# Kernel tuning notes

Measured on AMD Instinct MI355X. Metric: run time of the kernel, lower is better.

## Reference

```python
import jax, jax.numpy as jnp
import numpy as np

N, E, H = 100000, 640000, 64
DIN_N, DIN_E, L, OUT = 32, 16, 2, 1
BN_EPS = 1e-5


def setup_inputs() -> dict:
    key = jax.random.key(0)
    ks = iter(jax.random.split(key, 40))
    def p(shape, s=0.05):
        return jax.random.normal(next(ks), shape, dtype=jnp.float32) * s
    return {
        "x": jax.random.normal(next(ks), (N, DIN_N), dtype=jnp.float32),
        "edge_attr": jax.random.normal(next(ks), (E, DIN_E), dtype=jnp.float32),
        "src": jax.random.randint(next(ks), (E,), 0, N),
        "dst": jax.random.randint(next(ks), (E,), 0, N),
        "node_emb_w": p((DIN_N, H)), "node_emb_b": p((H,)),
        "edge_emb_w": p((DIN_E, H)), "edge_emb_b": p((H,)),
        "lin_edge_w": p((L, H, H)), "lin_edge_b": p((L, H)),
        "conv_w1": p((L, H, H)), "conv_b1": p((L, H)),
        "conv_w2": p((L, H, H)), "conv_b2": p((L, H)),
        "emlp_w1": p((L, 3 * H, H)), "emlp_b1": p((L, H)),
        "emlp_w2": p((L, H, H)), "emlp_b2": p((L, H)),
        "bn_gamma": jnp.ones((L, H), jnp.float32),
        "bn_beta": jnp.zeros((L, H), jnp.float32),
        "mlp_w1": p((3 * H, 50)), "mlp_b1": p((50,)),
        "mlp_w2": p((50, 25)), "mlp_b2": p((25,)),
        "mlp_w3": p((25, OUT)), "mlp_b3": p((OUT,)),
    }


def _batchnorm(h, gamma, beta):
    # training-mode BatchNorm1d over the node axis (biased variance)
    mu = jnp.mean(h, axis=0)
    var = jnp.mean(jnp.square(h - mu), axis=0)
    return gamma * (h - mu) * jax.lax.rsqrt(var + BN_EPS) + beta


def _forward(x, edge_attr, src, dst,
             node_emb_w, node_emb_b, edge_emb_w, edge_emb_b,
             lin_edge_w, lin_edge_b, conv_w1, conv_b1, conv_w2, conv_b2,
             emlp_w1, emlp_b1, emlp_w2, emlp_b2, bn_gamma, bn_beta,
             mlp_w1, mlp_b1, mlp_w2, mlp_b2, mlp_w3, mlp_b3):
    x = x @ node_emb_w + node_emb_b                       # [N, H]
    e = edge_attr @ edge_emb_w + edge_emb_b               # [E, H]
    for i in range(L):
        # GINEConv (eps=0): msg = ReLU(x_src + Lin(edge_attr)); sum at dst
        msg = jax.nn.relu(x[src] + e @ lin_edge_w[i] + lin_edge_b[i])
        agg = jax.ops.segment_sum(msg, dst, num_segments=N)
        h = x + agg
        h = jax.nn.relu(h @ conv_w1[i] + conv_b1[i]) @ conv_w2[i] + conv_b2[i]
        x = (x + jax.nn.relu(_batchnorm(h, bn_gamma[i], bn_beta[i]))) / 2
        cat = jnp.concatenate([x[src], x[dst], e], axis=-1)  # [E, 3H]
        upd = jax.nn.relu(cat @ emlp_w1[i] + emlp_b1[i]) @ emlp_w2[i] + emlp_b2[i]
        e = e + upd / 2
    # edge readout: relu(cat(x_src, x_dst)) ++ edge_attr -> MLP (dropout off/eval)
    er = jnp.concatenate(
        [jax.nn.relu(jnp.concatenate([x[src], x[dst]], axis=-1)), e], axis=-1)
    hmid = jax.nn.relu(er @ mlp_w1 + mlp_b1)
    hmid = jax.nn.relu(hmid @ mlp_w2 + mlp_b2)
    logit = hmid @ mlp_w3 + mlp_b3
    return x, logit


def reference(x, edge_attr, src, dst,
              node_emb_w, node_emb_b, edge_emb_w, edge_emb_b,
              lin_edge_w, lin_edge_b, conv_w1, conv_b1, conv_w2, conv_b2,
              emlp_w1, emlp_b1, emlp_w2, emlp_b2, bn_gamma, bn_beta,
              mlp_w1, mlp_b1, mlp_w2, mlp_b2, mlp_w3, mlp_b3):
    return _forward(x, edge_attr, src, dst,
                    node_emb_w, node_emb_b, edge_emb_w, edge_emb_b,
                    lin_edge_w, lin_edge_b, conv_w1, conv_b1, conv_w2, conv_b2,
                    emlp_w1, emlp_b1, emlp_w2, emlp_b2, bn_gamma, bn_beta,
                    mlp_w1, mlp_b1, mlp_w2, mlp_b2, mlp_w3, mlp_b3)
```

## Files before the change

kernel.cpp:

```cpp
#include <hip/hip_runtime.h>

#define NN 100000
#define NE 640000
#define NB_SCAN 98

typedef __attribute__((ext_vector_type(8))) short short8;
typedef __attribute__((ext_vector_type(4))) float f32x4;
typedef __attribute__((ext_vector_type(4))) ushort ushort4v;

__device__ __forceinline__ float bf2f(ushort u) {
    unsigned v = ((unsigned)u) << 16;
    return __builtin_bit_cast(float, v);
}
__device__ __forceinline__ ushort f2bf(float f) {
    unsigned u = __builtin_bit_cast(unsigned, f);
    u += 0x7fffu + ((u >> 16) & 1u);
    return (ushort)(u >> 16);
}
__device__ __forceinline__ short8 brelu(short8 v) {
    #pragma unroll
    for (int i = 0; i < 8; ++i) v[i] = (v[i] < (short)0) ? (short)0 : v[i];
    return v;
}

__global__ void k_hist(const int* __restrict__ dst, int* __restrict__ hist)
{
    int i = blockIdx.x * 256 + threadIdx.x;
    atomicAdd(&hist[dst[i]], 1);
}

__global__ __launch_bounds__(256) void k_scan_part(const int* __restrict__ hist,
                                                   int* __restrict__ rp,
                                                   int* __restrict__ parts)
{
    __shared__ int s[256];
    int b = blockIdx.x, t = threadIdx.x;
    int base = b * 1024 + t * 4;
    int v[4]; int sum = 0;
    #pragma unroll
    for (int i = 0; i < 4; ++i) { int idx = base + i; v[i] = (idx < NN) ? hist[idx] : 0; sum += v[i]; }
    s[t] = sum; __syncthreads();
    for (int off = 1; off < 256; off <<= 1) {
        int x = (t >= off) ? s[t - off] : 0;
        __syncthreads(); s[t] += x; __syncthreads();
    }
    int excl = s[t] - sum;
    if (t == 255) parts[b] = s[255];
    int run = excl;
    #pragma unroll
    for (int i = 0; i < 4; ++i) { int idx = base + i; if (idx < NN) rp[idx] = run; run += v[i]; }
}

__global__ void k_scan_tops(int* __restrict__ parts, int* __restrict__ rp)
{
    __shared__ int s[128];
    int t = threadIdx.x;
    int v = (t < NB_SCAN) ? parts[t] : 0;
    s[t] = v; __syncthreads();
    for (int off = 1; off < 128; off <<= 1) {
        int x = (t >= off) ? s[t - off] : 0;
        __syncthreads(); s[t] += x; __syncthreads();
    }
    parts[t] = s[t] - v;
    if (t == 0) rp[NN] = NE;
}

__global__ __launch_bounds__(256) void k_scan_add(int* __restrict__ rp,
                                                  const int* __restrict__ parts,
                                                  int* __restrict__ cursor)
{
    int i = blockIdx.x * 256 + threadIdx.x;
    if (i >= NN) return;
    int v = rp[i] + parts[i >> 10];
    rp[i] = v; cursor[i] = v;
}

__global__ void k_scatter(const int* __restrict__ dst,
                          int* __restrict__ cursor, int* __restrict__ eidx)
{
    int i = blockIdx.x * 256 + threadIdx.x;
    int d = dst[i];
    int p = atomicAdd(&cursor[d], 1);
    eidx[p] = i;
}

__global__ void k_w_subtile(const float* __restrict__ w, ushort* __restrict__ out,
                            int K, int Nin)
{
    int t = blockIdx.x * 256 + threadIdx.x;
    if (t >= K * 64) return;
    int k = t >> 6, c = t & 63;
    float v = (c < Nin) ? w[k * Nin + c] : 0.f;
    out[((k >> 3) * 64 + c) * 8 + (k & 7)] = f2bf(v);
}

__global__ void k_w_padk(const float* __restrict__ w, ushort* __restrict__ out,
                         int Kreal, int Kpad)
{
    int t = blockIdx.x * 256 + threadIdx.x;
    if (t >= Kpad * 64) return;
    int k = t >> 6, c = t & 63;
    float v = (k < Kreal) ? w[k * 64 + c] : 0.f;
    out[((k >> 3) * 64 + c) * 8 + (k & 7)] = f2bf(v);
}

__global__ void k_w_msg(const float* __restrict__ lw, ushort* __restrict__ out)
{
    int t = blockIdx.x * 256 + threadIdx.x;
    if (t >= 128 * 64) return;
    int k = t >> 6, c = t & 63;
    float v = (k < 64) ? (k == c ? 1.f : 0.f) : lw[(k - 64) * 64 + c];
    out[((k >> 3) * 64 + c) * 8 + (k & 7)] = f2bf(v);
}

__global__ __launch_bounds__(256) void k_node_emb_mfma(
    const float* __restrict__ xin, const ushort* __restrict__ ws,
    const float* __restrict__ b, float* __restrict__ xout,
    ushort* __restrict__ xb)
{
    __shared__ ushort wl[32 * 64];
    __shared__ float fbuf[4][16 * 64];
    __shared__ ushort bbuf[4][16 * 64];
    int tid = threadIdx.x;
    *(short8*)&wl[tid * 8] = *(const short8*)&ws[tid * 8];
    __syncthreads();

    int wid = tid >> 6, lane = tid & 63, c = lane & 15, kg = lane >> 4;
    int t = blockIdx.x * 4 + wid;
    if (t >= NN / 16) return;
    int n0 = t * 16;

    const float* xr = xin + (size_t)(n0 + c) * 32 + kg * 8;
    f32x4 u0 = *(const f32x4*)xr, u1 = *(const f32x4*)(xr + 4);
    short8 a;
    #pragma unroll
    for (int j = 0; j < 4; ++j) { a[j] = (short)f2bf(u0[j]); a[4 + j] = (short)f2bf(u1[j]); }

    f32x4 acc[4];
    #pragma unroll
    for (int nt = 0; nt < 4; ++nt) {
        float bv = b[nt * 16 + c];
        acc[nt] = f32x4{bv, bv, bv, bv};
        short8 bf = *(const short8*)&wl[(kg * 64 + nt * 16 + c) * 8];
        acc[nt] = __builtin_amdgcn_mfma_f32_16x16x32_bf16(a, bf, acc[nt], 0, 0, 0);
    }
    #pragma unroll
    for (int nt = 0; nt < 4; ++nt)
        #pragma unroll
        for (int i = 0; i < 4; ++i) {
            int rr = kg * 4 + i, cc = nt * 16 + c;
            float v = acc[nt][i];
            fbuf[wid][rr * 64 + cc] = v;
            bbuf[wid][rr * 64 + cc] = f2bf(v);
        }
    #pragma unroll
    for (int r = 0; r < 4; ++r) {
        int q = r * 64 + lane;
        *(f32x4*)&xout[(size_t)(n0 + (q >> 4)) * 64 + (q & 15) * 4] =
            *(f32x4*)&fbuf[wid][q * 4];
    }
    #pragma unroll
    for (int r = 0; r < 2; ++r) {
        int q = r * 64 + lane;
        *(short8*)&xb[(size_t)(n0 + (q >> 3)) * 64 + (q & 7) * 8] =
            *(short8*)&bbuf[wid][q * 8];
    }
}

__global__ __launch_bounds__(256) void k_edge_emb_fused(
    const float* __restrict__ ein, const ushort* __restrict__ ws,
    const float* __restrict__ b, ushort* __restrict__ eb,
    const ushort* __restrict__ xb, const int* __restrict__ src,
    const ushort* __restrict__ wm, const float* __restrict__ lb,
    ushort* __restrict__ msgbuf)
{
    __shared__ ushort wl[32 * 64];
    __shared__ ushort wml[128 * 64];
    __shared__ ushort bbuf[4][16 * 72];
    int tid = threadIdx.x;
    *(short8*)&wl[tid * 8] = *(const short8*)&ws[tid * 8];
    #pragma unroll
    for (int i = 0; i < 4; ++i)
        *(short8*)&wml[(i * 256 + tid) * 8] = *(const short8*)&wm[(i * 256 + tid) * 8];
    __syncthreads();

    int wid = tid >> 6, lane = tid & 63, c = lane & 15, kg = lane >> 4;
    int e0 = (blockIdx.x * 4 + wid) * 16;
    ushort* bb = bbuf[wid];

    const ushort* xs = xb + (size_t)src[e0 + c] * 64;
    short8 a0 = *(const short8*)(xs + kg * 8);
    short8 a1 = *(const short8*)(xs + 32 + kg * 8);

    short8 a = (short8)0;
    if (kg < 2) {
        const float* er = ein + (size_t)(e0 + c) * 16 + kg * 8;
        f32x4 u0 = *(const f32x4*)er, u1 = *(const f32x4*)(er + 4);
        #pragma unroll
        for (int j = 0; j < 4; ++j) { a[j] = (short)f2bf(u0[j]); a[4 + j] = (short)f2bf(u1[j]); }
    }
    f32x4 acc[4];
    #pragma unroll
    for (int nt = 0; nt < 4; ++nt) {
        float bv = b[nt * 16 + c];
        acc[nt] = f32x4{bv, bv, bv, bv};
        short8 bf = *(const short8*)&wl[(kg * 64 + nt * 16 + c) * 8];
        acc[nt] = __builtin_amdgcn_mfma_f32_16x16x32_bf16(a, bf, acc[nt], 0, 0, 0);
    }
    #pragma unroll
    for (int nt = 0; nt < 4; ++nt)
        #pragma unroll
        for (int i = 0; i < 4; ++i)
            bb[(kg * 4 + i) * 72 + nt * 16 + c] = f2bf(acc[nt][i]);
    #pragma unroll
    for (int r = 0; r < 2; ++r) {
        int q = r * 64 + lane;
        *(short8*)&eb[(size_t)(e0 + (q >> 3)) * 64 + (q & 7) * 8] =
            *(short8*)&bb[(q >> 3) * 72 + (q & 7) * 8];
    }
    short8 en0 = *(const short8*)&bb[c * 72 + kg * 8];
    short8 en1 = *(const short8*)&bb[c * 72 + 32 + kg * 8];

    f32x4 acc3[4];
    #pragma unroll
    for (int nt = 0; nt < 4; ++nt) {
        float bv = lb[nt * 16 + c];
        acc3[nt] = f32x4{bv, bv, bv, bv};
    }
    short8 af[4] = {a0, a1, en0, en1};
    #pragma unroll
    for (int ks = 0; ks < 4; ++ks) {
        #pragma unroll
        for (int nt = 0; nt < 4; ++nt) {
            short8 bf = *(const short8*)&wml[((ks * 4 + kg) * 64 + nt * 16 + c) * 8];
            acc3[nt] = __builtin_amdgcn_mfma_f32_16x16x32_bf16(af[ks], bf, acc3[nt], 0, 0, 0);
        }
    }
    #pragma unroll
    for (int nt = 0; nt < 4; ++nt)
        #pragma unroll
        for (int i = 0; i < 4; ++i)
            bb[(kg * 4 + i) * 72 + nt * 16 + c] = f2bf(fmaxf(acc3[nt][i], 0.f));
    #pragma unroll
    for (int r = 0; r < 2; ++r) {
        int q = r * 64 + lane;
        *(short8*)&msgbuf[(size_t)(e0 + (q >> 3)) * 64 + (q & 7) * 8] =
            *(short8*)&bb[(q >> 3) * 72 + (q & 7) * 8];
    }
}

__global__ __launch_bounds__(256) void k_conv_csr(
    const float* __restrict__ x, const ushort* __restrict__ msgbuf,
    const int* __restrict__ rp, const int* __restrict__ eidx,
    float* __restrict__ hout,
    const ushort* __restrict__ w1s, const float* __restrict__ b1,
    const ushort* __restrict__ w2s, const float* __restrict__ b2,
    float* __restrict__ stats)
{
    __shared__ ushort w1l[64 * 64];
    __shared__ ushort w2l[64 * 64];
    __shared__ ushort h1l[4][1024];
    __shared__ float red[2][4][64];
    int tid = threadIdx.x;
    #pragma unroll
    for (int i = 0; i < 2; ++i) {
        *(short8*)&w1l[(i * 256 + tid) * 8] = *(const short8*)&w1s[(i * 256 + tid) * 8];
        *(short8*)&w2l[(i * 256 + tid) * 8] = *(const short8*)&w2s[(i * 256 + tid) * 8];
    }
    __syncthreads();

    int wid = tid >> 6, lane = tid & 63;
    int c = lane & 15, kg = lane >> 4;

    short8 w2f[2][4];
    #pragma unroll
    for (int ks = 0; ks < 2; ++ks)
        #pragma unroll
        for (int nt = 0; nt < 4; ++nt)
            w2f[ks][nt] = *(const short8*)&w2l[((ks * 4 + kg) * 64 + nt * 16 + c) * 8];

    float b1v[4], b2v[4];
    #pragma unroll
    for (int nt = 0; nt < 4; ++nt) { b1v[nt] = b1[nt * 16 + c]; b2v[nt] = b2[nt * 16 + c]; }

    float s1[4] = {0.f, 0.f, 0.f, 0.f}, s2[4] = {0.f, 0.f, 0.f, 0.f};
    ushort* hl = h1l[wid];

    int t = blockIdx.x * 4 + wid;
    if (t < NN / 16) {
        int n0 = t * 16;
        int n = n0 + c;
        int jb = rp[n], je = rp[n + 1];
        float sm0[8] = {0,0,0,0,0,0,0,0}, sm1[8] = {0,0,0,0,0,0,0,0};
        if (jb < je) {
            int row = eidx[jb];
            short8 m0 = *(const short8*)&msgbuf[(size_t)row * 64 + kg * 8];
            short8 m1 = *(const short8*)&msgbuf[(size_t)row * 64 + 32 + kg * 8];
            for (int j = jb + 1; j <= je; ++j) {
                short8 p0, p1;
                if (j < je) {
                    int nrow = eidx[j];
                    p0 = *(const short8*)&msgbuf[(size_t)nrow * 64 + kg * 8];
                    p1 = *(const short8*)&msgbuf[(size_t)nrow * 64 + 32 + kg * 8];
                }
                #pragma unroll
                for (int i = 0; i < 8; ++i) {
                    sm0[i] += bf2f((ushort)m0[i]);
                    sm1[i] += bf2f((ushort)m1[i]);
                }
                if (j < je) { m0 = p0; m1 = p1; }
            }
        }
        const float* xr = x + (size_t)n * 64;
        f32x4 u0 = *(const f32x4*)(xr + kg * 8);
        f32x4 u1 = *(const f32x4*)(xr + kg * 8 + 4);
        f32x4 v0 = *(const f32x4*)(xr + 32 + kg * 8);
        f32x4 v1 = *(const f32x4*)(xr + 32 + kg * 8 + 4);
        short8 a[2];
        #pragma unroll
        for (int j = 0; j < 4; ++j) {
            a[0][j]     = (short)f2bf(u0[j] + sm0[j]);
            a[0][4 + j] = (short)f2bf(u1[j] + sm0[4 + j]);
            a[1][j]     = (short)f2bf(v0[j] + sm1[j]);
            a[1][4 + j] = (short)f2bf(v1[j] + sm1[4 + j]);
        }
        f32x4 acc[4];
        #pragma unroll
        for (int nt = 0; nt < 4; ++nt) acc[nt] = f32x4{b1v[nt], b1v[nt], b1v[nt], b1v[nt]};
        #pragma unroll
        for (int ks = 0; ks < 2; ++ks) {
            #pragma unroll
            for (int nt = 0; nt < 4; ++nt) {
                short8 bf = *(const short8*)&w1l[((ks * 4 + kg) * 64 + nt * 16 + c) * 8];
                acc[nt] = __builtin_amdgcn_mfma_f32_16x16x32_bf16(a[ks], bf, acc[nt], 0, 0, 0);
            }
        }
        #pragma unroll
        for (int nt = 0; nt < 4; ++nt) {
            #pragma unroll
            for (int i = 0; i < 4; ++i) {
                int rr = kg * 4 + i, cc = nt * 16 + c;
                hl[((cc >> 3) * 16 + rr) * 8 + (cc & 7)] = f2bf(fmaxf(acc[nt][i], 0.f));
            }
        }
        f32x4 acc2[4];
        #pragma unroll
        for (int nt = 0; nt < 4; ++nt) acc2[nt] = f32x4{b2v[nt], b2v[nt], b2v[nt], b2v[nt]};
        #pragma unroll
        for (int ks = 0; ks < 2; ++ks) {
            short8 ha = *(const short8*)&hl[((ks * 4 + kg) * 16 + c) * 8];
            #pragma unroll
            for (int nt = 0; nt < 4; ++nt)
                acc2[nt] = __builtin_amdgcn_mfma_f32_16x16x32_bf16(ha, w2f[ks][nt], acc2[nt], 0, 0, 0);
        }
        #pragma unroll
        for (int nt = 0; nt < 4; ++nt) {
            #pragma unroll
            for (int i = 0; i < 4; ++i) {
                int rr = kg * 4 + i, cc = nt * 16 + c;
                float h2 = acc2[nt][i];
                hout[(size_t)(n0 + rr) * 64 + cc] = h2;
                s1[nt] += h2;
                s2[nt] += h2 * h2;
            }
        }
    }
    #pragma unroll
    for (int nt = 0; nt < 4; ++nt) {
        float v1 = s1[nt], v2 = s2[nt];
        v1 += __shfl_xor(v1, 16); v1 += __shfl_xor(v1, 32);
        v2 += __shfl_xor(v2, 16); v2 += __shfl_xor(v2, 32);
        s1[nt] = v1; s2[nt] = v2;
    }
    if (lane < 16) {
        #pragma unroll
        for (int nt = 0; nt < 4; ++nt) {
            red[0][wid][nt * 16 + c] = s1[nt];
            red[1][wid][nt * 16 + c] = s2[nt];
        }
    }
    __syncthreads();
    if (wid == 0) {
        float a = red[0][0][lane] + red[0][1][lane] + red[0][2][lane] + red[0][3][lane];
        float b = red[1][0][lane] + red[1][1][lane] + red[1][2][lane] + red[1][3][lane];
        unsafeAtomicAdd(&stats[lane], a);
        unsafeAtomicAdd(&stats[64 + lane], b);
    }
}

__global__ void k_bnfin(float* __restrict__ stats,
                        const float* __restrict__ gamma,
                        const float* __restrict__ beta)
{
    int j = threadIdx.x;
    float mu = stats[j] * (1.f / NN);
    float var = stats[64 + j] * (1.f / NN) - mu * mu;
    float a = gamma[j] * rsqrtf(var + 1e-5f);
    stats[128 + j] = a;
    stats[192 + j] = beta[j] - mu * a;
}

__global__ __launch_bounds__(256) void k_xupd4(float* __restrict__ x,
                                               const float* __restrict__ h,
                                               const float* __restrict__ stats,
                                               ushort* __restrict__ xb)
{
    int idx = blockIdx.x * 256 + threadIdx.x;
    int j4 = (idx & 15) * 4;
    f32x4 hv = *(const f32x4*)&h[(size_t)idx * 4];
    f32x4 xv = *(const f32x4*)&x[(size_t)idx * 4];
    f32x4 av = *(const f32x4*)&stats[128 + j4];
    f32x4 cv = *(const f32x4*)&stats[192 + j4];
    f32x4 xo;
    ushort4v bo;
    #pragma unroll
    for (int i = 0; i < 4; ++i) {
        float r = fmaxf(fmaf(hv[i], av[i], cv[i]), 0.f);
        float xn = (xv[i] + r) * 0.5f;
        xo[i] = xn;
        bo[i] = f2bf(xn);
    }
    *(f32x4*)&x[(size_t)idx * 4] = xo;
    *(ushort4v*)&xb[(size_t)idx * 4] = bo;
}

template<int NEXT>
__global__ __launch_bounds__(256) void k_emlp_fused(
    const ushort* __restrict__ xb, ushort* __restrict__ eb,
    const int* __restrict__ src, const int* __restrict__ dst,
    const ushort* __restrict__ w1s, const float* __restrict__ b1,
    const ushort* __restrict__ w2s, const float* __restrict__ b2,
    const ushort* __restrict__ wm, const float* __restrict__ lbn,
    ushort* __restrict__ msgbuf)
{
    __shared__ ushort w1l[192 * 64];
    __shared__ ushort wml[NEXT ? 128 * 64 : 8];
    __shared__ ushort hb[4][1152];
    int tid = threadIdx.x;
    #pragma unroll
    for (int i = 0; i < 6; ++i)
        *(short8*)&w1l[(i * 256 + tid) * 8] = *(const short8*)&w1s[(i * 256 + tid) * 8];
    if (NEXT) {
        #pragma unroll
        for (int i = 0; i < 4; ++i)
            *(short8*)&wml[(i * 256 + tid) * 8] = *(const short8*)&wm[(i * 256 + tid) * 8];
    }
    __syncthreads();

    int wid = tid >> 6, lane = tid & 63;
    int c = lane & 15, kg = lane >> 4;

    short8 w2f[2][4];
    #pragma unroll
    for (int ks = 0; ks < 2; ++ks)
        #pragma unroll
        for (int nt = 0; nt < 4; ++nt)
            w2f[ks][nt] = *(const short8*)&w2s[((ks * 4 + kg) * 64 + nt * 16 + c) * 8];

    float b1v[4], b2v[4], lbv[4];
    #pragma unroll
    for (int nt = 0; nt < 4; ++nt) {
        b1v[nt] = b1[nt * 16 + c];
        b2v[nt] = b2[nt * 16 + c];
        lbv[nt] = NEXT ? lbn[nt * 16 + c] : 0.f;
    }
    ushort* hl = hb[wid];

    int ebase = blockIdx.x * 256 + wid * 64;

    short8 a[6];
    {
        int myedge = ebase + c;
        int s = src[myedge], d = dst[myedge];
        const ushort* xs = xb + (size_t)s * 64;
        const ushort* xd = xb + (size_t)d * 64;
        const ushort* ee = eb + (size_t)myedge * 64;
        a[0] = *(const short8*)(xs + kg * 8);
        a[1] = *(const short8*)(xs + 32 + kg * 8);
        a[2] = *(const short8*)(xd + kg * 8);
        a[3] = *(const short8*)(xd + 32 + kg * 8);
        a[4] = *(const short8*)(ee + kg * 8);
        a[5] = *(const short8*)(ee + 32 + kg * 8);
    }

    #pragma unroll 1
    for (int t4 = 0; t4 < 4; ++t4) {
        int e0 = ebase + t4 * 16;
        int myedge = e0 + c;

        short8 an[6];
        if (t4 < 3) {
            int sn = src[myedge + 16];
            int dn = dst[myedge + 16];
            const ushort* xsn = xb + (size_t)sn * 64;
            const ushort* xdn = xb + (size_t)dn * 64;
            const ushort* een = eb + (size_t)(myedge + 16) * 64;
            an[0] = *(const short8*)(xsn + kg * 8);
            an[1] = *(const short8*)(xsn + 32 + kg * 8);
            an[2] = *(const short8*)(xdn + kg * 8);
            an[3] = *(const short8*)(xdn + 32 + kg * 8);
            an[4] = *(const short8*)(een + kg * 8);
            an[5] = *(const short8*)(een + 32 + kg * 8);
        }

        f32x4 acc[4];
        #pragma unroll
        for (int nt = 0; nt < 4; ++nt) acc[nt] = f32x4{b1v[nt], b1v[nt], b1v[nt], b1v[nt]};
        #pragma unroll
        for (int ks = 0; ks < 6; ++ks) {
            #pragma unroll
            for (int nt = 0; nt < 4; ++nt) {
                short8 bf = *(const short8*)&w1l[((ks * 4 + kg) * 64 + nt * 16 + c) * 8];
                acc[nt] = __builtin_amdgcn_mfma_f32_16x16x32_bf16(a[ks], bf, acc[nt], 0, 0, 0);
            }
        }
        #pragma unroll
        for (int nt = 0; nt < 4; ++nt) {
            #pragma unroll
            for (int i = 0; i < 4; ++i) {
                int rr = kg * 4 + i, cc = nt * 16 + c;
                hl[((cc >> 3) * 16 + rr) * 8 + (cc & 7)] = f2bf(fmaxf(acc[nt][i], 0.f));
            }
        }
        f32x4 acc2[4];
        #pragma unroll
        for (int nt = 0; nt < 4; ++nt) acc2[nt] = f32x4{b2v[nt], b2v[nt], b2v[nt], b2v[nt]};
        #pragma unroll
        for (int ks = 0; ks < 2; ++ks) {
            short8 ha = *(const short8*)&hl[((ks * 4 + kg) * 16 + c) * 8];
            #pragma unroll
            for (int nt = 0; nt < 4; ++nt)
                acc2[nt] = __builtin_amdgcn_mfma_f32_16x16x32_bf16(ha, w2f[ks][nt], acc2[nt], 0, 0, 0);
        }
        #pragma unroll
        for (int nt = 0; nt < 4; ++nt)
            #pragma unroll
            for (int i = 0; i < 4; ++i)
                hl[(kg * 4 + i) * 72 + nt * 16 + c] = f2bf(acc2[nt][i]);
        short8 u0 = *(const short8*)&hl[c * 72 + kg * 8];
        short8 u1 = *(const short8*)&hl[c * 72 + 32 + kg * 8];
        short8 en0, en1;
        #pragma unroll
        for (int j = 0; j < 8; ++j) {
            en0[j] = (short)f2bf(bf2f((ushort)a[4][j]) + 0.5f * bf2f((ushort)u0[j]));
            en1[j] = (short)f2bf(bf2f((ushort)a[5][j]) + 0.5f * bf2f((ushort)u1[j]));
        }
        *(short8*)&eb[(size_t)myedge * 64 + kg * 8]      = en0;
        *(short8*)&eb[(size_t)myedge * 64 + 32 + kg * 8] = en1;

        if (NEXT) {
            f32x4 acc3[4];
            #pragma unroll
            for (int nt = 0; nt < 4; ++nt) acc3[nt] = f32x4{lbv[nt], lbv[nt], lbv[nt], lbv[nt]};
            short8 af[4] = {a[0], a[1], en0, en1};
            #pragma unroll
            for (int ks = 0; ks < 4; ++ks) {
                #pragma unroll
                for (int nt = 0; nt < 4; ++nt) {
                    short8 bf = *(const short8*)&wml[((ks * 4 + kg) * 64 + nt * 16 + c) * 8];
                    acc3[nt] = __builtin_amdgcn_mfma_f32_16x16x32_bf16(af[ks], bf, acc3[nt], 0, 0, 0);
                }
            }
            #pragma unroll
            for (int nt = 0; nt < 4; ++nt)
                #pragma unroll
                for (int i = 0; i < 4; ++i)
                    hl[(kg * 4 + i) * 72 + nt * 16 + c] = f2bf(fmaxf(acc3[nt][i], 0.f));
            #pragma unroll
            for (int r = 0; r < 2; ++r) {
                int q = r * 64 + lane;
                *(short8*)&msgbuf[(size_t)(e0 + (q >> 3)) * 64 + (q & 7) * 8] =
                    *(short8*)&hl[(q >> 3) * 72 + (q & 7) * 8];
            }
        }

        if (t4 < 3) {
            #pragma unroll
            for (int i = 0; i < 6; ++i) a[i] = an[i];
        }
    }
}

__global__ __launch_bounds__(256) void k_readout_mfma(
    const ushort* __restrict__ xb, const ushort* __restrict__ eb,
    const int* __restrict__ src, const int* __restrict__ dst,
    const ushort* __restrict__ w1s, const float* __restrict__ b1,
    const float* __restrict__ w2, const float* __restrict__ b2,
    const float* __restrict__ w3, const float* __restrict__ b3,
    float* __restrict__ logit)
{
    __shared__ ushort w1l[192 * 64];
    __shared__ ushort hw[4][64 * 50];
    int tid = threadIdx.x;
    #pragma unroll
    for (int i = 0; i < 6; ++i)
        *(short8*)&w1l[(i * 256 + tid) * 8] = *(const short8*)&w1s[(i * 256 + tid) * 8];
    __syncthreads();

    int wid = tid >> 6, lane = tid & 63;
    int c = lane & 15, kg = lane >> 4;
    float b1v[4];
    #pragma unroll
    for (int nt = 0; nt < 4; ++nt) b1v[nt] = (nt * 16 + c < 50) ? b1[nt * 16 + c] : 0.f;

    int ebase = blockIdx.x * 256 + wid * 64;

    short8 a[6];
    {
        int myedge = ebase + c;
        int s = src[myedge], d = dst[myedge];
        const ushort* xs = xb + (size_t)s * 64;
        const ushort* xd = xb + (size_t)d * 64;
        const ushort* ee = eb + (size_t)myedge * 64;
        a[0] = *(const short8*)(xs + kg * 8);
        a[1] = *(const short8*)(xs + 32 + kg * 8);
        a[2] = *(const short8*)(xd + kg * 8);
        a[3] = *(const short8*)(xd + 32 + kg * 8);
        a[4] = *(const short8*)(ee + kg * 8);
        a[5] = *(const short8*)(ee + 32 + kg * 8);
    }

    #pragma unroll 1
    for (int t4 = 0; t4 < 4; ++t4) {
        int e0 = ebase + t4 * 16;
        int myedge = e0 + c;

        short8 an[6];
        if (t4 < 3) {
            int sn = src[myedge + 16];
            int dn = dst[myedge + 16];
            const ushort* xsn = xb + (size_t)sn * 64;
            const ushort* xdn = xb + (size_t)dn * 64;
            const ushort* een = eb + (size_t)(myedge + 16) * 64;
            an[0] = *(const short8*)(xsn + kg * 8);
            an[1] = *(const short8*)(xsn + 32 + kg * 8);
            an[2] = *(const short8*)(xdn + kg * 8);
            an[3] = *(const short8*)(xdn + 32 + kg * 8);
            an[4] = *(const short8*)(een + kg * 8);
            an[5] = *(const short8*)(een + 32 + kg * 8);
        }

        short8 af[6];
        af[0] = brelu(a[0]); af[1] = brelu(a[1]);
        af[2] = brelu(a[2]); af[3] = brelu(a[3]);
        af[4] = a[4];        af[5] = a[5];

        f32x4 acc[4];
        #pragma unroll
        for (int nt = 0; nt < 4; ++nt) acc[nt] = f32x4{b1v[nt], b1v[nt], b1v[nt], b1v[nt]};
        #pragma unroll
        for (int ks = 0; ks < 6; ++ks) {
            #pragma unroll
            for (int nt = 0; nt < 4; ++nt) {
                short8 bf = *(const short8*)&w1l[((ks * 4 + kg) * 64 + nt * 16 + c) * 8];
                acc[nt] = __builtin_amdgcn_mfma_f32_16x16x32_bf16(af[ks], bf, acc[nt], 0, 0, 0);
            }
        }
        #pragma unroll
        for (int nt = 0; nt < 4; ++nt) {
            #pragma unroll
            for (int i = 0; i < 4; ++i) {
                int rr = kg * 4 + i, cc = nt * 16 + c;
                if (cc < 50)
                    hw[wid][(t4 * 16 + rr) * 50 + cc] = f2bf(fmaxf(acc[nt][i], 0.f));
            }
        }
        if (t4 < 3) {
            #pragma unroll
            for (int i = 0; i < 6; ++i) a[i] = an[i];
        }
    }
    int edge = blockIdx.x * 256 + wid * 64 + lane;
    const ushort* hrow = &hw[wid][lane * 50];
    float a25[25];
    #pragma unroll
    for (int j = 0; j < 25; ++j) a25[j] = b2[j];
    #pragma unroll 2
    for (int k = 0; k < 50; ++k) {
        float hv = bf2f(hrow[k]);
        #pragma unroll
        for (int j = 0; j < 25; ++j) a25[j] = fmaf(hv, w2[k * 25 + j], a25[j]);
    }
    float lg = b3[0];
    #pragma unroll
    for (int k = 0; k < 25; ++k) lg = fmaf(fmaxf(a25[k], 0.f), w3[k], lg);
    logit[edge] = lg;
}

extern "C" void kernel_launch(void* const* d_in, const int* in_sizes, int n_in,
                              void* d_out, int out_size, void* d_ws, size_t ws_size,
                              hipStream_t stream)
{
    const float* x_in  = (const float*)d_in[0];
    const float* eattr = (const float*)d_in[1];
    const int*   src   = (const int*)d_in[2];
    const int*   dst   = (const int*)d_in[3];
    const float* n_w   = (const float*)d_in[4];
    const float* n_b   = (const float*)d_in[5];
    const float* e_w   = (const float*)d_in[6];
    const float* e_b   = (const float*)d_in[7];
    const float* lw    = (const float*)d_in[8];
    const float* lb    = (const float*)d_in[9];
    const float* cw1   = (const float*)d_in[10];
    const float* cb1   = (const float*)d_in[11];
    const float* cw2   = (const float*)d_in[12];
    const float* cb2   = (const float*)d_in[13];
    const float* ew1   = (const float*)d_in[14];
    const float* eb1   = (const float*)d_in[15];
    const float* ew2   = (const float*)d_in[16];
    const float* eb2   = (const float*)d_in[17];
    const float* gam   = (const float*)d_in[18];
    const float* bet   = (const float*)d_in[19];
    const float* m1w   = (const float*)d_in[20];
    const float* m1b   = (const float*)d_in[21];
    const float* m2w   = (const float*)d_in[22];
    const float* m2b   = (const float*)d_in[23];
    const float* m3w   = (const float*)d_in[24];
    const float* m3b   = (const float*)d_in[25];

    float* xbuf  = (float*)d_out;
    float* logit = xbuf + (size_t)NN * 64;

    ushort* eb     = (ushort*)d_ws;
    float*  tmp    = (float*)(eb + (size_t)NE * 64);
    float*  stats  = tmp + (size_t)NN * 64;
    ushort* w1s    = (ushort*)(stats + 256);
    ushort* w2s    = w1s + 2 * 192 * 64;
    ushort* m1s    = w2s + 2 * 64 * 64;
    ushort* xb     = m1s + 192 * 64;
    ushort* wms    = xb + (size_t)NN * 64;
    ushort* cw1s   = wms + 2 * 128 * 64;
    ushort* cw2s   = cw1s + 2 * 64 * 64;
    ushort* nws    = cw2s + 2 * 64 * 64;
    ushort* ews    = nws + 32 * 64;
    ushort* msgbuf = ews + 32 * 64;
    int*    hist   = (int*)(msgbuf + (size_t)NE * 64);
    int*    rp     = hist + NN;
    int*    cursor = rp + NN + 1;
    int*    parts  = cursor + NN;
    int*    eidx   = parts + 128;

    hipMemsetAsync(hist, 0, NN * sizeof(int), stream);
    k_hist<<<NE / 256, 256, 0, stream>>>(dst, hist);
    k_scan_part<<<NB_SCAN, 256, 0, stream>>>(hist, rp, parts);
    k_scan_tops<<<1, 128, 0, stream>>>(parts, rp);
    k_scan_add<<<(NN + 255) / 256, 256, 0, stream>>>(rp, parts, cursor);
    k_scatter<<<NE / 256, 256, 0, stream>>>(dst, cursor, eidx);

    k_w_subtile<<<48, 256, 0, stream>>>(ew1,            w1s,            192, 64);
    k_w_subtile<<<48, 256, 0, stream>>>(ew1 + 192 * 64, w1s + 192 * 64, 192, 64);
    k_w_subtile<<<16, 256, 0, stream>>>(ew2,            w2s,            64, 64);
    k_w_subtile<<<16, 256, 0, stream>>>(ew2 + 64 * 64,  w2s + 64 * 64,  64, 64);
    k_w_subtile<<<48, 256, 0, stream>>>(m1w,            m1s,            192, 50);
    k_w_msg<<<32, 256, 0, stream>>>(lw,           wms);
    k_w_msg<<<32, 256, 0, stream>>>(lw + 64 * 64, wms + 128 * 64);
    k_w_subtile<<<16, 256, 0, stream>>>(cw1,            cw1s,           64, 64);
    k_w_subtile<<<16, 256, 0, stream>>>(cw1 + 64 * 64,  cw1s + 64 * 64, 64, 64);
    k_w_subtile<<<16, 256, 0, stream>>>(cw2,            cw2s,           64, 64);
    k_w_subtile<<<16, 256, 0, stream>>>(cw2 + 64 * 64,  cw2s + 64 * 64, 64, 64);
    k_w_padk<<<8, 256, 0, stream>>>(n_w, nws, 32, 32);
    k_w_padk<<<8, 256, 0, stream>>>(e_w, ews, 16, 32);

    k_node_emb_mfma<<<(NN / 16 + 3) / 4, 256, 0, stream>>>(x_in, nws, n_b, xbuf, xb);
    k_edge_emb_fused<<<NE / 64, 256, 0, stream>>>(eattr, ews, e_b, eb,
                                                  xb, src, wms, lb, msgbuf);

    for (int l = 0; l < 2; ++l) {
        hipMemsetAsync(stats, 0, 256 * sizeof(float), stream);
        k_conv_csr<<<(NN / 16 + 3) / 4, 256, 0, stream>>>(
            xbuf, msgbuf, rp, eidx, tmp, cw1s + l * 64 * 64, cb1 + l * 64,
            cw2s + l * 64 * 64, cb2 + l * 64, stats);
        k_bnfin<<<1, 64, 0, stream>>>(stats, gam + l * 64, bet + l * 64);
        k_xupd4<<<NN * 16 / 256, 256, 0, stream>>>(xbuf, tmp, stats, xb);
        if (l == 0) {
            k_emlp_fused<1><<<NE / 256, 256, 0, stream>>>(
                xb, eb, src, dst, w1s, eb1, w2s, eb2,
                wms + 128 * 64, lb + 64, msgbuf);
        } else {
            k_emlp_fused<0><<<NE / 256, 256, 0, stream>>>(
                xb, eb, src, dst, w1s + 192 * 64, eb1 + 64, w2s + 64 * 64, eb2 + 64,
                wms, lb, msgbuf);
        }
    }

    k_readout_mfma<<<NE / 256, 256, 0, stream>>>(xb, eb, src, dst,
                                                 m1s, m1b, m2w, m2b, m3w, m3b, logit);
}
```

Measured before the change: 536.7 us.

## Fuse second-layer edge MLP update into the edge readout kernel

```diff
diff --git a/kernel.cpp b/kernel.cpp
--- a/kernel.cpp
+++ b/kernel.cpp
@@ -424,8 +424,7 @@
     *(ushort4v*)&xb[(size_t)idx * 4] = bo;
 }
 
-template<int NEXT>
-__global__ __launch_bounds__(256) void k_emlp_fused(
+__global__ __launch_bounds__(256) void k_emlp_fused1(
     const ushort* __restrict__ xb, ushort* __restrict__ eb,
     const int* __restrict__ src, const int* __restrict__ dst,
     const ushort* __restrict__ w1s, const float* __restrict__ b1,
@@ -434,17 +433,15 @@
     ushort* __restrict__ msgbuf)
 {
     __shared__ ushort w1l[192 * 64];
-    __shared__ ushort wml[NEXT ? 128 * 64 : 8];
+    __shared__ ushort wml[128 * 64];
     __shared__ ushort hb[4][1152];
     int tid = threadIdx.x;
     #pragma unroll
     for (int i = 0; i < 6; ++i)
         *(short8*)&w1l[(i * 256 + tid) * 8] = *(const short8*)&w1s[(i * 256 + tid) * 8];
-    if (NEXT) {
-        #pragma unroll
-        for (int i = 0; i < 4; ++i)
-            *(short8*)&wml[(i * 256 + tid) * 8] = *(const short8*)&wm[(i * 256 + tid) * 8];
-    }
+    #pragma unroll
+    for (int i = 0; i < 4; ++i)
+        *(short8*)&wml[(i * 256 + tid) * 8] = *(const short8*)&wm[(i * 256 + tid) * 8];
     __syncthreads();
 
     int wid = tid >> 6, lane = tid & 63;
@@ -462,7 +459,7 @@
     for (int nt = 0; nt < 4; ++nt) {
         b1v[nt] = b1[nt * 16 + c];
         b2v[nt] = b2[nt * 16 + c];
-        lbv[nt] = NEXT ? lbn[nt * 16 + c] : 0.f;
+        lbv[nt] = lbn[nt * 16 + c];
     }
     ushort* hl = hb[wid];
 
@@ -548,30 +545,28 @@
         *(short8*)&eb[(size_t)myedge * 64 + kg * 8]      = en0;
         *(short8*)&eb[(size_t)myedge * 64 + 32 + kg * 8] = en1;
 
-        if (NEXT) {
-            f32x4 acc3[4];
-            #pragma unroll
-            for (int nt = 0; nt < 4; ++nt) acc3[nt] = f32x4{lbv[nt], lbv[nt], lbv[nt], lbv[nt]};
-            short8 af[4] = {a[0], a[1], en0, en1};
-            #pragma unroll
-            for (int ks = 0; ks < 4; ++ks) {
-                #pragma unroll
-                for (int nt = 0; nt < 4; ++nt) {
-                    short8 bf = *(const short8*)&wml[((ks * 4 + kg) * 64 + nt * 16 + c) * 8];
-                    acc3[nt] = __builtin_amdgcn_mfma_f32_16x16x32_bf16(af[ks], bf, acc3[nt], 0, 0, 0);
-                }
-            }
-            #pragma unroll
-            for (int nt = 0; nt < 4; ++nt)
-                #pragma unroll
-                for (int i = 0; i < 4; ++i)
-                    hl[(kg * 4 + i) * 72 + nt * 16 + c] = f2bf(fmaxf(acc3[nt][i], 0.f));
-            #pragma unroll
-            for (int r = 0; r < 2; ++r) {
-                int q = r * 64 + lane;
-                *(short8*)&msgbuf[(size_t)(e0 + (q >> 3)) * 64 + (q & 7) * 8] =
-                    *(short8*)&hl[(q >> 3) * 72 + (q & 7) * 8];
-            }
+        f32x4 acc3[4];
+        #pragma unroll
+        for (int nt = 0; nt < 4; ++nt) acc3[nt] = f32x4{lbv[nt], lbv[nt], lbv[nt], lbv[nt]};
+        short8 af[4] = {a[0], a[1], en0, en1};
+        #pragma unroll
+        for (int ks = 0; ks < 4; ++ks) {
+            #pragma unroll
+            for (int nt = 0; nt < 4; ++nt) {
+                short8 bf = *(const short8*)&wml[((ks * 4 + kg) * 64 + nt * 16 + c) * 8];
+                acc3[nt] = __builtin_amdgcn_mfma_f32_16x16x32_bf16(af[ks], bf, acc3[nt], 0, 0, 0);
+            }
+        }
+        #pragma unroll
+        for (int nt = 0; nt < 4; ++nt)
+            #pragma unroll
+            for (int i = 0; i < 4; ++i)
+                hl[(kg * 4 + i) * 72 + nt * 16 + c] = f2bf(fmaxf(acc3[nt][i], 0.f));
+        #pragma unroll
+        for (int r = 0; r < 2; ++r) {
+            int q = r * 64 + lane;
+            *(short8*)&msgbuf[(size_t)(e0 + (q >> 3)) * 64 + (q & 7) * 8] =
+                *(short8*)&hl[(q >> 3) * 72 + (q & 7) * 8];
         }
 
         if (t4 < 3) {
@@ -581,15 +576,18 @@
     }
 }
 
-__global__ __launch_bounds__(256) void k_readout_mfma(
-    const ushort* __restrict__ xb, const ushort* __restrict__ eb,
+__global__ __launch_bounds__(256) void k_emlp_rd(
+    const ushort* __restrict__ xb, ushort* __restrict__ eb,
     const int* __restrict__ src, const int* __restrict__ dst,
     const ushort* __restrict__ w1s, const float* __restrict__ b1,
-    const float* __restrict__ w2, const float* __restrict__ b2,
-    const float* __restrict__ w3, const float* __restrict__ b3,
+    const ushort* __restrict__ w2s, const float* __restrict__ b2,
+    const ushort* __restrict__ m1s, const float* __restrict__ m1b,
+    const float* __restrict__ m2w, const float* __restrict__ m2b,
+    const float* __restrict__ m3w, const float* __restrict__ m3b,
     float* __restrict__ logit)
 {
     __shared__ ushort w1l[192 * 64];
+    __shared__ ushort hb[4][1152];
     __shared__ ushort hw[4][64 * 50];
     int tid = threadIdx.x;
     #pragma unroll
@@ -599,9 +597,22 @@
 
     int wid = tid >> 6, lane = tid & 63;
     int c = lane & 15, kg = lane >> 4;
-    float b1v[4];
-    #pragma unroll
-    for (int nt = 0; nt < 4; ++nt) b1v[nt] = (nt * 16 + c < 50) ? b1[nt * 16 + c] : 0.f;
+
+    short8 w2f[2][4];
+    #pragma unroll
+    for (int ks = 0; ks < 2; ++ks)
+        #pragma unroll
+        for (int nt = 0; nt < 4; ++nt)
+            w2f[ks][nt] = *(const short8*)&w2s[((ks * 4 + kg) * 64 + nt * 16 + c) * 8];
+
+    float b1v[4], b2v[4], b1r[4];
+    #pragma unroll
+    for (int nt = 0; nt < 4; ++nt) {
+        b1v[nt] = b1[nt * 16 + c];
+        b2v[nt] = b2[nt * 16 + c];
+        b1r[nt] = (nt * 16 + c < 50) ? m1b[nt * 16 + c] : 0.f;
+    }
+    ushort* hl = hb[wid];
 
     int ebase = blockIdx.x * 256 + wid * 64;
 
@@ -640,11 +651,6 @@
             an[5] = *(const short8*)(een + 32 + kg * 8);
         }
 
-        short8 af[6];
-        af[0] = brelu(a[0]); af[1] = brelu(a[1]);
-        af[2] = brelu(a[2]); af[3] = brelu(a[3]);
-        af[4] = a[4];        af[5] = a[5];
-
         f32x4 acc[4];
         #pragma unroll
         for (int nt = 0; nt < 4; ++nt) acc[nt] = f32x4{b1v[nt], b1v[nt], b1v[nt], b1v[nt]};
@@ -653,7 +659,56 @@
             #pragma unroll
             for (int nt = 0; nt < 4; ++nt) {
                 short8 bf = *(const short8*)&w1l[((ks * 4 + kg) * 64 + nt * 16 + c) * 8];
-                acc[nt] = __builtin_amdgcn_mfma_f32_16x16x32_bf16(af[ks], bf, acc[nt], 0, 0, 0);
+                acc[nt] = __builtin_amdgcn_mfma_f32_16x16x32_bf16(a[ks], bf, acc[nt], 0, 0, 0);
+            }
+        }
+        #pragma unroll
+        for (int nt = 0; nt < 4; ++nt) {
+            #pragma unroll
+            for (int i = 0; i < 4; ++i) {
+                int rr = kg * 4 + i, cc = nt * 16 + c;
+                hl[((cc >> 3) * 16 + rr) * 8 + (cc & 7)] = f2bf(fmaxf(acc[nt][i], 0.f));
+            }
+        }
+        f32x4 acc2[4];
+        #pragma unroll
+        for (int nt = 0; nt < 4; ++nt) acc2[nt] = f32x4{b2v[nt], b2v[nt], b2v[nt], b2v[nt]};
+        #pragma unroll
+        for (int ks = 0; ks < 2; ++ks) {
+            short8 ha = *(const short8*)&hl[((ks * 4 + kg) * 16 + c) * 8];
+            #pragma unroll
+            for (int nt = 0; nt < 4; ++nt)
+                acc2[nt] = __builtin_amdgcn_mfma_f32_16x16x32_bf16(ha, w2f[ks][nt], acc2[nt], 0, 0, 0);
+        }
+        #pragma unroll
+        for (int nt = 0; nt < 4; ++nt)
+            #pragma unroll
+            for (int i = 0; i < 4; ++i)
+                hl[(kg * 4 + i) * 72 + nt * 16 + c] = f2bf(acc2[nt][i]);
+        short8 u0 = *(const short8*)&hl[c * 72 + kg * 8];
+        short8 u1 = *(const short8*)&hl[c * 72 + 32 + kg * 8];
+        short8 en0, en1;
+        #pragma unroll
+        for (int j = 0; j < 8; ++j) {
+            en0[j] = (short)f2bf(bf2f((ushort)a[4][j]) + 0.5f * bf2f((ushort)u0[j]));
+            en1[j] = (short)f2bf(bf2f((ushort)a[5][j]) + 0.5f * bf2f((ushort)u1[j]));
+        }
+        *(short8*)&eb[(size_t)myedge * 64 + kg * 8]      = en0;
+        *(short8*)&eb[(size_t)myedge * 64 + 32 + kg * 8] = en1;
+
+        f32x4 accr[4];
+        #pragma unroll
+        for (int nt = 0; nt < 4; ++nt) accr[nt] = f32x4{b1r[nt], b1r[nt], b1r[nt], b1r[nt]};
+        short8 ar[6];
+        ar[0] = brelu(a[0]); ar[1] = brelu(a[1]);
+        ar[2] = brelu(a[2]); ar[3] = brelu(a[3]);
+        ar[4] = en0;         ar[5] = en1;
+        #pragma unroll
+        for (int ks = 0; ks < 6; ++ks) {
+            #pragma unroll
+            for (int nt = 0; nt < 4; ++nt) {
+                short8 bf = *(const short8*)&m1s[((ks * 4 + kg) * 64 + nt * 16 + c) * 8];
+                accr[nt] = __builtin_amdgcn_mfma_f32_16x16x32_bf16(ar[ks], bf, accr[nt], 0, 0, 0);
             }
         }
         #pragma unroll
@@ -662,28 +717,30 @@
             for (int i = 0; i < 4; ++i) {
                 int rr = kg * 4 + i, cc = nt * 16 + c;
                 if (cc < 50)
-                    hw[wid][(t4 * 16 + rr) * 50 + cc] = f2bf(fmaxf(acc[nt][i], 0.f));
-            }
-        }
+                    hw[wid][(t4 * 16 + rr) * 50 + cc] = f2bf(fmaxf(accr[nt][i], 0.f));
+            }
+        }
+
         if (t4 < 3) {
             #pragma unroll
             for (int i = 0; i < 6; ++i) a[i] = an[i];
         }
     }
-    int edge = blockIdx.x * 256 + wid * 64 + lane;
+
+    int edge = ebase + lane;
     const ushort* hrow = &hw[wid][lane * 50];
     float a25[25];
     #pragma unroll
-    for (int j = 0; j < 25; ++j) a25[j] = b2[j];
+    for (int j = 0; j < 25; ++j) a25[j] = m2b[j];
     #pragma unroll 2
     for (int k = 0; k < 50; ++k) {
         float hv = bf2f(hrow[k]);
         #pragma unroll
-        for (int j = 0; j < 25; ++j) a25[j] = fmaf(hv, w2[k * 25 + j], a25[j]);
-    }
-    float lg = b3[0];
-    #pragma unroll
-    for (int k = 0; k < 25; ++k) lg = fmaf(fmaxf(a25[k], 0.f), w3[k], lg);
+        for (int j = 0; j < 25; ++j) a25[j] = fmaf(hv, m2w[k * 25 + j], a25[j]);
+    }
+    float lg = m3b[0];
+    #pragma unroll
+    for (int k = 0; k < 25; ++k) lg = fmaf(fmaxf(a25[k], 0.f), m3w[k], lg);
     logit[edge] = lg;
 }
 
@@ -765,24 +822,22 @@
     k_edge_emb_fused<<<NE / 64, 256, 0, stream>>>(eattr, ews, e_b, eb,
                                                   xb, src, wms, lb, msgbuf);
 
-    for (int l = 0; l < 2; ++l) {
-        hipMemsetAsync(stats, 0, 256 * sizeof(float), stream);
-        k_conv_csr<<<(NN / 16 + 3) / 4, 256, 0, stream>>>(
-            xbuf, msgbuf, rp, eidx, tmp, cw1s + l * 64 * 64, cb1 + l * 64,
-            cw2s + l * 64 * 64, cb2 + l * 64, stats);
-        k_bnfin<<<1, 64, 0, stream>>>(stats, gam + l * 64, bet + l * 64);
-        k_xupd4<<<NN * 16 / 256, 256, 0, stream>>>(xbuf, tmp, stats, xb);
-        if (l == 0) {
-            k_emlp_fused<1><<<NE / 256, 256, 0, stream>>>(
-                xb, eb, src, dst, w1s, eb1, w2s, eb2,
-                wms + 128 * 64, lb + 64, msgbuf);
-        } else {
-            k_emlp_fused<0><<<NE / 256, 256, 0, stream>>>(
-                xb, eb, src, dst, w1s + 192 * 64, eb1 + 64, w2s + 64 * 64, eb2 + 64,
-                wms, lb, msgbuf);
-        }
-    }
-
-    k_readout_mfma<<<NE / 256, 256, 0, stream>>>(xb, eb, src, dst,
-                                                 m1s, m1b, m2w, m2b, m3w, m3b, logit);
-}
+    hipMemsetAsync(stats, 0, 256 * sizeof(float), stream);
+    k_conv_csr<<<(NN / 16 + 3) / 4, 256, 0, stream>>>(
+        xbuf, msgbuf, rp, eidx, tmp, cw1s, cb1, cw2s, cb2, stats);
+    k_bnfin<<<1, 64, 0, stream>>>(stats, gam, bet);
+    k_xupd4<<<NN * 16 / 256, 256, 0, stream>>>(xbuf, tmp, stats, xb);
+    k_emlp_fused1<<<NE / 256, 256, 0, stream>>>(
+        xb, eb, src, dst, w1s, eb1, w2s, eb2,
+        wms + 128 * 64, lb + 64, msgbuf);
+
+    hipMemsetAsync(stats, 0, 256 * sizeof(float), stream);
+    k_conv_csr<<<(NN / 16 + 3) / 4, 256, 0, stream>>>(
+        xbuf, msgbuf, rp, eidx, tmp, cw1s + 64 * 64, cb1 + 64,
+        cw2s + 64 * 64, cb2 + 64, stats);
+    k_bnfin<<<1, 64, 0, stream>>>(stats, gam + 64, bet + 64);
+    k_xupd4<<<NN * 16 / 256, 256, 0, stream>>>(xbuf, tmp, stats, xb);
+    k_emlp_rd<<<NE / 256, 256, 0, stream>>>(
+        xb, eb, src, dst, w1s + 192 * 64, eb1 + 64, w2s + 64 * 64, eb2 + 64,
+        m1s, m1b, m2w, m2b, m3w, m3b, logit);
+}
```

Result: slower. 570.4 us (+6.3%).
